# Kernel optimization log

Measured on AMD Instinct MI355X. Metric: run time of the kernel, lower is better.

Reference implementation:

```python
import jax, jax.numpy as jnp
import numpy as np

B, T, U, H = 4, 256, 64, 512
INNER, VOCAB = 512, 1024


def setup_inputs() -> dict:
    key = jax.random.key(0)
    ks = jax.random.split(key, 6)
    s_in = 1.0 / np.sqrt(2 * H)
    s_h = 1.0 / np.sqrt(INNER)
    return {
        "enc_state": jax.random.normal(ks[0], (B, T, H), dtype=jnp.float32),
        "dec_state": jax.random.normal(ks[1], (B, U, H), dtype=jnp.float32),
        "W1": jax.random.normal(ks[2], (2 * H, INNER), dtype=jnp.float32) * s_in,
        "b1": jnp.zeros((INNER,), dtype=jnp.float32),
        "W2": jax.random.normal(ks[3], (INNER, VOCAB), dtype=jnp.float32) * s_h,
        "b2": jnp.zeros((VOCAB,), dtype=jnp.float32),
    }


def reference(enc_state, dec_state, W1, b1, W2, b2):
    # JointNet: broadcast enc [B,T,1,H] and dec [B,1,U,H], concat -> Linear -> tanh -> Linear -> log_softmax
    # concat+Linear is split into two smaller matmuls (mathematically identical):
    # cat([e,d]) @ W1 == e @ W1[:H] + d @ W1[H:]
    enc_proj = jnp.einsum("bth,hi->bti", enc_state, W1[:H])      # [B,T,INNER]
    dec_proj = jnp.einsum("buh,hi->bui", dec_state, W1[H:])      # [B,U,INNER]
    hidden = jnp.tanh(enc_proj[:, :, None, :] + dec_proj[:, None, :, :] + b1)  # [B,T,U,INNER]
    logits = jnp.einsum("btui,iv->btuv", hidden, W2) + b2        # [B,T,U,VOCAB]
    return jax.nn.log_softmax(logits, axis=-1)
```

## Files before the change

kernel.cpp:

```cpp
#include <hip/hip_runtime.h>
#include <hip/hip_bf16.h>
#include <cstdint>
#include <cstddef>


typedef __attribute__((ext_vector_type(8))) short short8;
typedef __attribute__((ext_vector_type(4))) float f32x4;

#define AS_STRIDE 520
#define SMEM_A_BYTES (64 * AS_STRIDE * 2)
#define SMEM_BS_OFF SMEM_A_BYTES
#define BS_CHUNK 65536
#define SMEM_RED_OFF (SMEM_BS_OFF + BS_CHUNK)
#define SMEM_TOTAL (SMEM_RED_OFF + 16 * 64 * 4 * 2)

#define WS_EP_OFF 0
#define WS_DP_OFF (1024 * 512 * 4)
#define WS_W2_OFF (WS_DP_OFF + 256 * 512 * 4)

__device__ __forceinline__ unsigned short f2bf(float x) {
  unsigned int u = __builtin_bit_cast(unsigned int, x);
  u += 0x7FFFu + ((u >> 16) & 1u);
  return (unsigned short)(u >> 16);
}

__device__ __forceinline__ float fast_tanh(float x) {
  float ax = fabsf(x);
  float e = __expf(-2.0f * ax);
  float t = (1.0f - e) / (1.0f + e);
  return copysignf(t, x);
}

__device__ __forceinline__ void gload_lds16(const void* g, void* l) {
  __builtin_amdgcn_global_load_lds(
      (const __attribute__((address_space(1))) unsigned int*)g,
      (__attribute__((address_space(3))) unsigned int*)l, 16, 0, 0);
}

__global__ __launch_bounds__(512) void prep_proj(
    const float* __restrict__ enc, const float* __restrict__ dec,
    const float* __restrict__ W1, const float* __restrict__ b1,
    float* __restrict__ ep, float* __restrict__ dp) {
  __shared__ float As[4 * 512];
  const int tid = threadIdx.x;
  const int r0 = blockIdx.x * 4;
  const bool isenc = (r0 < 1024);
  const float* A = isenc ? (enc + (size_t)r0 * 512) : (dec + (size_t)(r0 - 1024) * 512);
  const float* W = isenc ? W1 : (W1 + 512 * 512);
  float* O = isenc ? (ep + (size_t)r0 * 512) : (dp + (size_t)(r0 - 1024) * 512);

  for (int idx = tid; idx < 4 * 512; idx += 512) As[idx] = A[idx];
  __syncthreads();

  const int c = tid;
  float acc[4] = {0.f, 0.f, 0.f, 0.f};
  const float4* As4 = (const float4*)As;
#pragma unroll 4
  for (int k4 = 0; k4 < 128; ++k4) {
    const int kb = k4 * 4;
    float w0 = W[(size_t)(kb + 0) * 512 + c];
    float w1 = W[(size_t)(kb + 1) * 512 + c];
    float w2 = W[(size_t)(kb + 2) * 512 + c];
    float w3 = W[(size_t)(kb + 3) * 512 + c];
#pragma unroll
    for (int r = 0; r < 4; ++r) {
      float4 a = As4[r * 128 + k4];
      acc[r] += a.x * w0 + a.y * w1 + a.z * w2 + a.w * w3;
    }
  }
  const float bias = isenc ? b1[c] : 0.0f;
#pragma unroll
  for (int r = 0; r < 4; ++r) O[(size_t)r * 512 + c] = acc[r] + bias;
}

__global__ __launch_bounds__(256) void prep_w2(const float* __restrict__ W2,
                                               char* __restrict__ w2st) {
  const int g = blockIdx.x * 256 + threadIdx.x;
  const int v = g & 1023;
  const int kc = g >> 10;
  unsigned short vals[32];
#pragma unroll
  for (int ki = 0; ki < 32; ++ki)
    vals[ki] = f2bf(W2[(size_t)(kc * 32 + ki) * 1024 + v]);
  uint4* dst = (uint4*)(w2st + (size_t)kc * BS_CHUNK + (size_t)v * 64);
  const uint4* s = (const uint4*)vals;
  dst[0] = s[0]; dst[1] = s[1]; dst[2] = s[2]; dst[3] = s[3];
}

__global__ __launch_bounds__(1024, 1) void joint(
    const float* __restrict__ ep, const float* __restrict__ dp,
    const char* __restrict__ w2st, const float* __restrict__ b2,
    float* __restrict__ out) {
  extern __shared__ char smem[];
  unsigned short* As = (unsigned short*)smem;
  char* Bs = smem + SMEM_BS_OFF;
  float* redM = (float*)(smem + SMEM_RED_OFF);
  float* redS = redM + 16 * 64;

  const int tid = threadIdx.x;
  const int wave = tid >> 6, lane = tid & 63;
  const int lo = lane & 15, hi = lane >> 4;
  const int wm = wave >> 3, wn = wave & 7;
  const int bt = blockIdx.x;
  const int m0 = bt * 64;
  const int dpbase = (bt >> 8) * 64;

  {
    const char* src = w2st;
#pragma unroll
    for (int r = 0; r < 4; ++r) {
      const int off = r * 16384 + tid * 16;
      gload_lds16(src + off, Bs + off);
    }
  }

  {
    const int c = tid & 511;
    const int rh = tid >> 9;
    const float e = ep[(size_t)bt * 512 + c];
#pragma unroll 4
    for (int r = 0; r < 32; ++r) {
      const int row = rh * 32 + r;
      float h = fast_tanh(e + dp[(size_t)(dpbase + row) * 512 + c]);
      As[row * AS_STRIDE + c] = f2bf(h);
    }
  }

  f32x4 acc[2][8];
#pragma unroll
  for (int mi = 0; mi < 2; ++mi)
#pragma unroll
    for (int ni = 0; ni < 8; ++ni)
#pragma unroll
      for (int j = 0; j < 4; ++j) acc[mi][ni][j] = 0.0f;

  const int nbase = wn * 128;
  const int arow0 = wm * 32 + lo;

  for (int kc = 0; kc < 16; ++kc) {
    __syncthreads();
    short8 a0 = *(const short8*)(As + (size_t)arow0 * AS_STRIDE + kc * 32 + hi * 8);
    short8 a1 = *(const short8*)(As + (size_t)(arow0 + 16) * AS_STRIDE + kc * 32 + hi * 8);
#pragma unroll
    for (int ni = 0; ni < 8; ++ni) {
      short8 b = *(const short8*)(Bs + (size_t)(nbase + ni * 16 + lo) * 64 + hi * 16);
      acc[0][ni] = __builtin_amdgcn_mfma_f32_16x16x32_bf16(a0, b, acc[0][ni], 0, 0, 0);
      acc[1][ni] = __builtin_amdgcn_mfma_f32_16x16x32_bf16(a1, b, acc[1][ni], 0, 0, 0);
    }
    if (kc < 15) {
      __syncthreads();
      const char* src = w2st + (size_t)(kc + 1) * BS_CHUNK;
#pragma unroll
      for (int r = 0; r < 4; ++r) {
        const int off = r * 16384 + tid * 16;
        gload_lds16(src + off, Bs + off);
      }
    }
  }
  __syncthreads();

  float b2v[8];
#pragma unroll
  for (int ni = 0; ni < 8; ++ni) b2v[ni] = b2[nbase + ni * 16 + lo];
#pragma unroll
  for (int mi = 0; mi < 2; ++mi)
#pragma unroll
    for (int ni = 0; ni < 8; ++ni)
#pragma unroll
      for (int j = 0; j < 4; ++j) acc[mi][ni][j] += b2v[ni];

  float pm[2][4];
#pragma unroll
  for (int mi = 0; mi < 2; ++mi)
#pragma unroll
    for (int r = 0; r < 4; ++r) {
      float m = -3.402823e38f;
#pragma unroll
      for (int ni = 0; ni < 8; ++ni) m = fmaxf(m, acc[mi][ni][r]);
      pm[mi][r] = m;
    }
#pragma unroll
  for (int off = 1; off < 16; off <<= 1)
#pragma unroll
    for (int mi = 0; mi < 2; ++mi)
#pragma unroll
      for (int r = 0; r < 4; ++r)
        pm[mi][r] = fmaxf(pm[mi][r], __shfl_xor(pm[mi][r], off));
  if (lo == 0) {
#pragma unroll
    for (int mi = 0; mi < 2; ++mi)
#pragma unroll
      for (int r = 0; r < 4; ++r)
        redM[wave * 64 + wm * 32 + mi * 16 + hi * 4 + r] = pm[mi][r];
  }
  __syncthreads();
  float rm[2][4];
#pragma unroll
  for (int mi = 0; mi < 2; ++mi)
#pragma unroll
    for (int r = 0; r < 4; ++r) {
      const int gr = wm * 32 + mi * 16 + hi * 4 + r;
      float m = redM[(wm * 8 + 0) * 64 + gr];
#pragma unroll
      for (int w = 1; w < 8; ++w) m = fmaxf(m, redM[(wm * 8 + w) * 64 + gr]);
      rm[mi][r] = m;
    }

  float ps[2][4];
#pragma unroll
  for (int mi = 0; mi < 2; ++mi)
#pragma unroll
    for (int r = 0; r < 4; ++r) {
      float s = 0.0f;
#pragma unroll
      for (int ni = 0; ni < 8; ++ni) s += __expf(acc[mi][ni][r] - rm[mi][r]);
      ps[mi][r] = s;
    }
#pragma unroll
  for (int off = 1; off < 16; off <<= 1)
#pragma unroll
    for (int mi = 0; mi < 2; ++mi)
#pragma unroll
      for (int r = 0; r < 4; ++r)
        ps[mi][r] += __shfl_xor(ps[mi][r], off);
  if (lo == 0) {
#pragma unroll
    for (int mi = 0; mi < 2; ++mi)
#pragma unroll
      for (int r = 0; r < 4; ++r)
        redS[wave * 64 + wm * 32 + mi * 16 + hi * 4 + r] = ps[mi][r];
  }
  __syncthreads();

#pragma unroll
  for (int mi = 0; mi < 2; ++mi)
#pragma unroll
    for (int r = 0; r < 4; ++r) {
      const int gr = wm * 32 + mi * 16 + hi * 4 + r;
      float s = 0.0f;
#pragma unroll
      for (int w = 0; w < 8; ++w) s += redS[(wm * 8 + w) * 64 + gr];
      const float sub = rm[mi][r] + __logf(s);
      float* op = out + (size_t)(m0 + gr) * 1024 + nbase + lo;
#pragma unroll
      for (int ni = 0; ni < 8; ++ni) op[ni * 16] = acc[mi][ni][r] - sub;
    }
}

extern "C" void kernel_launch(void* const* d_in, const int* in_sizes, int n_in,
                              void* d_out, int out_size, void* d_ws, size_t ws_size,
                              hipStream_t stream) {
  const float* enc = (const float*)d_in[0];
  const float* dec = (const float*)d_in[1];
  const float* W1  = (const float*)d_in[2];
  const float* b1  = (const float*)d_in[3];
  const float* W2  = (const float*)d_in[4];
  const float* b2  = (const float*)d_in[5];
  float* out = (float*)d_out;

  char* ws = (char*)d_ws;
  float* ep = (float*)(ws + WS_EP_OFF);
  float* dp = (float*)(ws + WS_DP_OFF);
  char* w2st = ws + WS_W2_OFF;

  prep_proj<<<320, 512, 0, stream>>>(enc, dec, W1, b1, ep, dp);
  prep_w2<<<64, 256, 0, stream>>>(W2, w2st);
  joint<<<1024, 1024, SMEM_TOTAL, stream>>>(ep, dp, w2st, b2, out);
}
```

Baseline: 215.1 us.

## Register double-buffer W2 chunks in joint kernel and merge prep kernels

The joint kernel stops using direct global-to-LDS loads. It keeps two W2 chunks in registers, prefetching chunk k+2 while chunk k is written to LDS and consumed by MFMAs, and raises wave priority during the MFMA block. The two prep kernels are merged into one launch with a block-index split, removing one kernel launch. This costs more VGPRs (32 extra registers per thread at 1024 threads/block) and adds an LDS store pass, but it should hide global latency better than the previous load-then-barrier scheme.

```diff
diff --git a/kernel.cpp b/kernel.cpp
--- a/kernel.cpp
+++ b/kernel.cpp
@@ -31,60 +31,54 @@
   return copysignf(t, x);
 }
 
-__device__ __forceinline__ void gload_lds16(const void* g, void* l) {
-  __builtin_amdgcn_global_load_lds(
-      (const __attribute__((address_space(1))) unsigned int*)g,
-      (__attribute__((address_space(3))) unsigned int*)l, 16, 0, 0);
-}
-
-__global__ __launch_bounds__(512) void prep_proj(
+__global__ __launch_bounds__(512) void prep(
     const float* __restrict__ enc, const float* __restrict__ dec,
     const float* __restrict__ W1, const float* __restrict__ b1,
-    float* __restrict__ ep, float* __restrict__ dp) {
+    const float* __restrict__ W2,
+    float* __restrict__ ep, float* __restrict__ dp, char* __restrict__ w2st) {
   __shared__ float As[4 * 512];
   const int tid = threadIdx.x;
-  const int r0 = blockIdx.x * 4;
-  const bool isenc = (r0 < 1024);
-  const float* A = isenc ? (enc + (size_t)r0 * 512) : (dec + (size_t)(r0 - 1024) * 512);
-  const float* W = isenc ? W1 : (W1 + 512 * 512);
-  float* O = isenc ? (ep + (size_t)r0 * 512) : (dp + (size_t)(r0 - 1024) * 512);
-
-  for (int idx = tid; idx < 4 * 512; idx += 512) As[idx] = A[idx];
-  __syncthreads();
-
-  const int c = tid;
-  float acc[4] = {0.f, 0.f, 0.f, 0.f};
-  const float4* As4 = (const float4*)As;
+  if (blockIdx.x < 320) {
+    const int r0 = blockIdx.x * 4;
+    const bool isenc = (r0 < 1024);
+    const float* A = isenc ? (enc + (size_t)r0 * 512) : (dec + (size_t)(r0 - 1024) * 512);
+    const float* W = isenc ? W1 : (W1 + 512 * 512);
+    float* O = isenc ? (ep + (size_t)r0 * 512) : (dp + (size_t)(r0 - 1024) * 512);
+
+    for (int idx = tid; idx < 4 * 512; idx += 512) As[idx] = A[idx];
+    __syncthreads();
+
+    const int c = tid;
+    float acc[4] = {0.f, 0.f, 0.f, 0.f};
+    const float4* As4 = (const float4*)As;
 #pragma unroll 4
-  for (int k4 = 0; k4 < 128; ++k4) {
-    const int kb = k4 * 4;
-    float w0 = W[(size_t)(kb + 0) * 512 + c];
-    float w1 = W[(size_t)(kb + 1) * 512 + c];
-    float w2 = W[(size_t)(kb + 2) * 512 + c];
-    float w3 = W[(size_t)(kb + 3) * 512 + c];
-#pragma unroll
-    for (int r = 0; r < 4; ++r) {
-      float4 a = As4[r * 128 + k4];
-      acc[r] += a.x * w0 + a.y * w1 + a.z * w2 + a.w * w3;
-    }
-  }
-  const float bias = isenc ? b1[c] : 0.0f;
-#pragma unroll
-  for (int r = 0; r < 4; ++r) O[(size_t)r * 512 + c] = acc[r] + bias;
-}
-
-__global__ __launch_bounds__(256) void prep_w2(const float* __restrict__ W2,
-                                               char* __restrict__ w2st) {
-  const int g = blockIdx.x * 256 + threadIdx.x;
-  const int v = g & 1023;
-  const int kc = g >> 10;
-  unsigned short vals[32];
-#pragma unroll
-  for (int ki = 0; ki < 32; ++ki)
-    vals[ki] = f2bf(W2[(size_t)(kc * 32 + ki) * 1024 + v]);
-  uint4* dst = (uint4*)(w2st + (size_t)kc * BS_CHUNK + (size_t)v * 64);
-  const uint4* s = (const uint4*)vals;
-  dst[0] = s[0]; dst[1] = s[1]; dst[2] = s[2]; dst[3] = s[3];
+    for (int k4 = 0; k4 < 128; ++k4) {
+      const int kb = k4 * 4;
+      float w0 = W[(size_t)(kb + 0) * 512 + c];
+      float w1 = W[(size_t)(kb + 1) * 512 + c];
+      float w2 = W[(size_t)(kb + 2) * 512 + c];
+      float w3 = W[(size_t)(kb + 3) * 512 + c];
+#pragma unroll
+      for (int r = 0; r < 4; ++r) {
+        float4 a = As4[r * 128 + k4];
+        acc[r] += a.x * w0 + a.y * w1 + a.z * w2 + a.w * w3;
+      }
+    }
+    const float bias = isenc ? b1[c] : 0.0f;
+#pragma unroll
+    for (int r = 0; r < 4; ++r) O[(size_t)r * 512 + c] = acc[r] + bias;
+  } else {
+    const int g = (blockIdx.x - 320) * 512 + tid;
+    const int v = g & 1023;
+    const int kc = g >> 10;
+    unsigned short vals[32];
+#pragma unroll
+    for (int ki = 0; ki < 32; ++ki)
+      vals[ki] = f2bf(W2[(size_t)(kc * 32 + ki) * 1024 + v]);
+    uint4* dst = (uint4*)(w2st + (size_t)kc * BS_CHUNK + (size_t)v * 64);
+    const uint4* s = (const uint4*)vals;
+    dst[0] = s[0]; dst[1] = s[1]; dst[2] = s[2]; dst[3] = s[3];
+  }
 }
 
 __global__ __launch_bounds__(1024, 1) void joint(
@@ -105,13 +99,18 @@
   const int m0 = bt * 64;
   const int dpbase = (bt >> 8) * 64;
 
+  uint4 P0, P1, P2, P3, Q0, Q1, Q2, Q3;
   {
-    const char* src = w2st;
-#pragma unroll
-    for (int r = 0; r < 4; ++r) {
-      const int off = r * 16384 + tid * 16;
-      gload_lds16(src + off, Bs + off);
-    }
+    const char* s0 = w2st;
+    const char* s1 = w2st + BS_CHUNK;
+    P0 = *(const uint4*)(s0 + 0 * 16384 + tid * 16);
+    P1 = *(const uint4*)(s0 + 1 * 16384 + tid * 16);
+    P2 = *(const uint4*)(s0 + 2 * 16384 + tid * 16);
+    P3 = *(const uint4*)(s0 + 3 * 16384 + tid * 16);
+    Q0 = *(const uint4*)(s1 + 0 * 16384 + tid * 16);
+    Q1 = *(const uint4*)(s1 + 1 * 16384 + tid * 16);
+    Q2 = *(const uint4*)(s1 + 2 * 16384 + tid * 16);
+    Q3 = *(const uint4*)(s1 + 3 * 16384 + tid * 16);
   }
 
   {
@@ -137,26 +136,48 @@
   const int nbase = wn * 128;
   const int arow0 = wm * 32 + lo;
 
-  for (int kc = 0; kc < 16; ++kc) {
-    __syncthreads();
-    short8 a0 = *(const short8*)(As + (size_t)arow0 * AS_STRIDE + kc * 32 + hi * 8);
-    short8 a1 = *(const short8*)(As + (size_t)(arow0 + 16) * AS_STRIDE + kc * 32 + hi * 8);
-#pragma unroll
-    for (int ni = 0; ni < 8; ++ni) {
-      short8 b = *(const short8*)(Bs + (size_t)(nbase + ni * 16 + lo) * 64 + hi * 16);
-      acc[0][ni] = __builtin_amdgcn_mfma_f32_16x16x32_bf16(a0, b, acc[0][ni], 0, 0, 0);
-      acc[1][ni] = __builtin_amdgcn_mfma_f32_16x16x32_bf16(a1, b, acc[1][ni], 0, 0, 0);
-    }
-    if (kc < 15) {
-      __syncthreads();
-      const char* src = w2st + (size_t)(kc + 1) * BS_CHUNK;
-#pragma unroll
-      for (int r = 0; r < 4; ++r) {
-        const int off = r * 16384 + tid * 16;
-        gload_lds16(src + off, Bs + off);
-      }
-    }
-  }
+  __syncthreads();
+
+#define K_STEP(S0, S1, S2, S3, KC, PF, NEXT)                                        \
+  {                                                                                 \
+    __builtin_amdgcn_s_barrier();              \
+    asm volatile("" ::: "memory");                                                  \
+    *(uint4*)(Bs + 0 * 16384 + tid * 16) = S0;     \
+    *(uint4*)(Bs + 1 * 16384 + tid * 16) = S1;                                      \
+    *(uint4*)(Bs + 2 * 16384 + tid * 16) = S2;                                      \
+    *(uint4*)(Bs + 3 * 16384 + tid * 16) = S3;                                      \
+    if (PF) {                                                                       \
+      const char* _src = w2st + (size_t)(NEXT)*BS_CHUNK;                            \
+      S0 = *(const uint4*)(_src + 0 * 16384 + tid * 16);                            \
+      S1 = *(const uint4*)(_src + 1 * 16384 + tid * 16);                            \
+      S2 = *(const uint4*)(_src + 2 * 16384 + tid * 16);                            \
+      S3 = *(const uint4*)(_src + 3 * 16384 + tid * 16);                            \
+    }                                                                               \
+    asm volatile("s_waitcnt lgkmcnt(0)" ::: "memory");  \
+    __builtin_amdgcn_s_barrier();                    \
+    asm volatile("" ::: "memory");                                                  \
+    __builtin_amdgcn_sched_barrier(0);                                              \
+    short8 a0 = *(const short8*)(As + (size_t)arow0 * AS_STRIDE + (KC)*32 + hi * 8);\
+    short8 a1 = *(const short8*)(As + (size_t)(arow0 + 16) * AS_STRIDE + (KC)*32 + hi * 8); \
+    __builtin_amdgcn_s_setprio(1);                                                  \
+    _Pragma("unroll")                                                               \
+    for (int ni = 0; ni < 8; ++ni) {                                                \
+      short8 b = *(const short8*)(Bs + (size_t)(nbase + ni * 16 + lo) * 64 + hi * 16); \
+      acc[0][ni] = __builtin_amdgcn_mfma_f32_16x16x32_bf16(a0, b, acc[0][ni], 0, 0, 0); \
+      acc[1][ni] = __builtin_amdgcn_mfma_f32_16x16x32_bf16(a1, b, acc[1][ni], 0, 0, 0); \
+    }                                                                               \
+    __builtin_amdgcn_s_setprio(0);                                                  \
+  }
+
+  for (int kc2 = 0; kc2 < 7; ++kc2) {
+    const int kc = kc2 * 2;
+    K_STEP(P0, P1, P2, P3, kc, 1, kc + 2);
+    K_STEP(Q0, Q1, Q2, Q3, kc + 1, 1, kc + 3);
+  }
+  K_STEP(P0, P1, P2, P3, 14, 0, 0);
+  K_STEP(Q0, Q1, Q2, Q3, 15, 0, 0);
+#undef K_STEP
+
   __syncthreads();
 
   float b2v[8];
@@ -263,7 +284,6 @@
   float* dp = (float*)(ws + WS_DP_OFF);
   char* w2st = ws + WS_W2_OFF;
 
-  prep_proj<<<320, 512, 0, stream>>>(enc, dec, W1, b1, ep, dp);
-  prep_w2<<<64, 256, 0, stream>>>(W2, w2st);
+  prep<<<352, 512, 0, stream>>>(enc, dec, W1, b1, W2, ep, dp, w2st);
   joint<<<1024, 1024, SMEM_TOTAL, stream>>>(ep, dp, w2st, b2, out);
 }
```

New measurement: 198.6 us. -7.7%, faster.

## Load W2 fragments straight to registers with prefetch, halve joint tile, merge prep kernels

Applied to the files above, without the earlier changes.

The joint kernel no longer stages W2 chunks through LDS with block-wide barriers. Each wave now loads its bf16 W2 fragments directly from global memory into registers and prefetches the next K chunk during the current MFMAs. Blocks shrink to 512 threads covering 32 rows, which cuts LDS use enough to allow several resident blocks per CU, and setprio is raised around the MFMA burst. The two prep kernels are merged into one launch. In exchange, every block re-reads all of W2 from global memory or cache, and register pressure rises from the double-buffered B fragments.

```diff
diff --git a/kernel.cpp b/kernel.cpp
--- a/kernel.cpp
+++ b/kernel.cpp
@@ -8,11 +8,7 @@
 typedef __attribute__((ext_vector_type(4))) float f32x4;
 
 #define AS_STRIDE 520
-#define SMEM_A_BYTES (64 * AS_STRIDE * 2)
-#define SMEM_BS_OFF SMEM_A_BYTES
 #define BS_CHUNK 65536
-#define SMEM_RED_OFF (SMEM_BS_OFF + BS_CHUNK)
-#define SMEM_TOTAL (SMEM_RED_OFF + 16 * 64 * 4 * 2)
 
 #define WS_EP_OFF 0
 #define WS_DP_OFF (1024 * 512 * 4)
@@ -31,98 +27,86 @@
   return copysignf(t, x);
 }
 
-__device__ __forceinline__ void gload_lds16(const void* g, void* l) {
-  __builtin_amdgcn_global_load_lds(
-      (const __attribute__((address_space(1))) unsigned int*)g,
-      (__attribute__((address_space(3))) unsigned int*)l, 16, 0, 0);
-}
-
-__global__ __launch_bounds__(512) void prep_proj(
+__global__ __launch_bounds__(512) void prep(
     const float* __restrict__ enc, const float* __restrict__ dec,
     const float* __restrict__ W1, const float* __restrict__ b1,
-    float* __restrict__ ep, float* __restrict__ dp) {
+    const float* __restrict__ W2,
+    float* __restrict__ ep, float* __restrict__ dp, char* __restrict__ w2st) {
   __shared__ float As[4 * 512];
   const int tid = threadIdx.x;
-  const int r0 = blockIdx.x * 4;
-  const bool isenc = (r0 < 1024);
-  const float* A = isenc ? (enc + (size_t)r0 * 512) : (dec + (size_t)(r0 - 1024) * 512);
-  const float* W = isenc ? W1 : (W1 + 512 * 512);
-  float* O = isenc ? (ep + (size_t)r0 * 512) : (dp + (size_t)(r0 - 1024) * 512);
-
-  for (int idx = tid; idx < 4 * 512; idx += 512) As[idx] = A[idx];
-  __syncthreads();
-
-  const int c = tid;
-  float acc[4] = {0.f, 0.f, 0.f, 0.f};
-  const float4* As4 = (const float4*)As;
+  if (blockIdx.x < 320) {
+    const int r0 = blockIdx.x * 4;
+    const bool isenc = (r0 < 1024);
+    const float* A = isenc ? (enc + (size_t)r0 * 512) : (dec + (size_t)(r0 - 1024) * 512);
+    const float* W = isenc ? W1 : (W1 + 512 * 512);
+    float* O = isenc ? (ep + (size_t)r0 * 512) : (dp + (size_t)(r0 - 1024) * 512);
+
+    for (int idx = tid; idx < 4 * 512; idx += 512) As[idx] = A[idx];
+    __syncthreads();
+
+    const int c = tid;
+    float acc[4] = {0.f, 0.f, 0.f, 0.f};
+    const float4* As4 = (const float4*)As;
 #pragma unroll 4
-  for (int k4 = 0; k4 < 128; ++k4) {
-    const int kb = k4 * 4;
-    float w0 = W[(size_t)(kb + 0) * 512 + c];
-    float w1 = W[(size_t)(kb + 1) * 512 + c];
-    float w2 = W[(size_t)(kb + 2) * 512 + c];
-    float w3 = W[(size_t)(kb + 3) * 512 + c];
-#pragma unroll
-    for (int r = 0; r < 4; ++r) {
-      float4 a = As4[r * 128 + k4];
-      acc[r] += a.x * w0 + a.y * w1 + a.z * w2 + a.w * w3;
-    }
-  }
-  const float bias = isenc ? b1[c] : 0.0f;
-#pragma unroll
-  for (int r = 0; r < 4; ++r) O[(size_t)r * 512 + c] = acc[r] + bias;
-}
-
-__global__ __launch_bounds__(256) void prep_w2(const float* __restrict__ W2,
-                                               char* __restrict__ w2st) {
-  const int g = blockIdx.x * 256 + threadIdx.x;
-  const int v = g & 1023;
-  const int kc = g >> 10;
-  unsigned short vals[32];
-#pragma unroll
-  for (int ki = 0; ki < 32; ++ki)
-    vals[ki] = f2bf(W2[(size_t)(kc * 32 + ki) * 1024 + v]);
-  uint4* dst = (uint4*)(w2st + (size_t)kc * BS_CHUNK + (size_t)v * 64);
-  const uint4* s = (const uint4*)vals;
-  dst[0] = s[0]; dst[1] = s[1]; dst[2] = s[2]; dst[3] = s[3];
-}
-
-__global__ __launch_bounds__(1024, 1) void joint(
+    for (int k4 = 0; k4 < 128; ++k4) {
+      const int kb = k4 * 4;
+      float w0 = W[(size_t)(kb + 0) * 512 + c];
+      float w1 = W[(size_t)(kb + 1) * 512 + c];
+      float w2 = W[(size_t)(kb + 2) * 512 + c];
+      float w3 = W[(size_t)(kb + 3) * 512 + c];
+#pragma unroll
+      for (int r = 0; r < 4; ++r) {
+        float4 a = As4[r * 128 + k4];
+        acc[r] += a.x * w0 + a.y * w1 + a.z * w2 + a.w * w3;
+      }
+    }
+    const float bias = isenc ? b1[c] : 0.0f;
+#pragma unroll
+    for (int r = 0; r < 4; ++r) O[(size_t)r * 512 + c] = acc[r] + bias;
+  } else {
+    const int g = (blockIdx.x - 320) * 512 + tid;
+    const int v = g & 1023;
+    const int kc = g >> 10;
+    unsigned short vals[32];
+#pragma unroll
+    for (int ki = 0; ki < 32; ++ki)
+      vals[ki] = f2bf(W2[(size_t)(kc * 32 + ki) * 1024 + v]);
+    uint4* dst = (uint4*)(w2st + (size_t)kc * BS_CHUNK + (size_t)v * 64);
+    const uint4* s = (const uint4*)vals;
+    dst[0] = s[0]; dst[1] = s[1]; dst[2] = s[2]; dst[3] = s[3];
+  }
+}
+
+__global__ __launch_bounds__(512, 4) void joint(
     const float* __restrict__ ep, const float* __restrict__ dp,
     const char* __restrict__ w2st, const float* __restrict__ b2,
     float* __restrict__ out) {
-  extern __shared__ char smem[];
-  unsigned short* As = (unsigned short*)smem;
-  char* Bs = smem + SMEM_BS_OFF;
-  float* redM = (float*)(smem + SMEM_RED_OFF);
-  float* redS = redM + 16 * 64;
+  __shared__ unsigned short As[32 * AS_STRIDE];
+  __shared__ float redM[8 * 32];
+  __shared__ float redS[8 * 32];
 
   const int tid = threadIdx.x;
   const int wave = tid >> 6, lane = tid & 63;
   const int lo = lane & 15, hi = lane >> 4;
-  const int wm = wave >> 3, wn = wave & 7;
-  const int bt = blockIdx.x;
-  const int m0 = bt * 64;
-  const int dpbase = (bt >> 8) * 64;
+  const int m0 = blockIdx.x * 32;
+  const int bt = m0 >> 6;
+  const int dprow0 = ((bt >> 8) << 6) + (m0 & 63);
+  const int nbase = wave * 128;
+
+  const char* bbase = w2st + (size_t)(nbase + lo) * 64 + hi * 16;
+
+  short8 b[8];
+#pragma unroll
+  for (int ni = 0; ni < 8; ++ni)
+    b[ni] = *(const short8*)(bbase + ni * 1024);
 
   {
-    const char* src = w2st;
-#pragma unroll
-    for (int r = 0; r < 4; ++r) {
-      const int off = r * 16384 + tid * 16;
-      gload_lds16(src + off, Bs + off);
-    }
-  }
-
-  {
-    const int c = tid & 511;
-    const int rh = tid >> 9;
+    const int c = tid;
     const float e = ep[(size_t)bt * 512 + c];
 #pragma unroll 4
     for (int r = 0; r < 32; ++r) {
-      const int row = rh * 32 + r;
-      float h = fast_tanh(e + dp[(size_t)(dpbase + row) * 512 + c]);
-      As[row * AS_STRIDE + c] = f2bf(h);
+      float h = fast_tanh(e + dp[(size_t)(dprow0 + r) * 512 + c]);
+      As[r * AS_STRIDE + c] = f2bf(h);
     }
   }
 
@@ -134,30 +118,31 @@
 #pragma unroll
       for (int j = 0; j < 4; ++j) acc[mi][ni][j] = 0.0f;
 
-  const int nbase = wn * 128;
-  const int arow0 = wm * 32 + lo;
-
+  __syncthreads();
+
+#pragma unroll
   for (int kc = 0; kc < 16; ++kc) {
-    __syncthreads();
-    short8 a0 = *(const short8*)(As + (size_t)arow0 * AS_STRIDE + kc * 32 + hi * 8);
-    short8 a1 = *(const short8*)(As + (size_t)(arow0 + 16) * AS_STRIDE + kc * 32 + hi * 8);
+    short8 bn[8];
+    if (kc < 15) {
+      const char* src = bbase + (size_t)(kc + 1) * BS_CHUNK;
+#pragma unroll
+      for (int ni = 0; ni < 8; ++ni)
+        bn[ni] = *(const short8*)(src + ni * 1024);
+    }
+    short8 a0 = *(const short8*)(As + (size_t)lo * AS_STRIDE + kc * 32 + hi * 8);
+    short8 a1 = *(const short8*)(As + (size_t)(16 + lo) * AS_STRIDE + kc * 32 + hi * 8);
+    __builtin_amdgcn_s_setprio(1);
 #pragma unroll
     for (int ni = 0; ni < 8; ++ni) {
-      short8 b = *(const short8*)(Bs + (size_t)(nbase + ni * 16 + lo) * 64 + hi * 16);
-      acc[0][ni] = __builtin_amdgcn_mfma_f32_16x16x32_bf16(a0, b, acc[0][ni], 0, 0, 0);
-      acc[1][ni] = __builtin_amdgcn_mfma_f32_16x16x32_bf16(a1, b, acc[1][ni], 0, 0, 0);
-    }
+      acc[0][ni] = __builtin_amdgcn_mfma_f32_16x16x32_bf16(a0, b[ni], acc[0][ni], 0, 0, 0);
+      acc[1][ni] = __builtin_amdgcn_mfma_f32_16x16x32_bf16(a1, b[ni], acc[1][ni], 0, 0, 0);
+    }
+    __builtin_amdgcn_s_setprio(0);
     if (kc < 15) {
-      __syncthreads();
-      const char* src = w2st + (size_t)(kc + 1) * BS_CHUNK;
-#pragma unroll
-      for (int r = 0; r < 4; ++r) {
-        const int off = r * 16384 + tid * 16;
-        gload_lds16(src + off, Bs + off);
-      }
-    }
-  }
-  __syncthreads();
+#pragma unroll
+      for (int ni = 0; ni < 8; ++ni) b[ni] = bn[ni];
+    }
+  }
 
   float b2v[8];
 #pragma unroll
@@ -191,7 +176,7 @@
     for (int mi = 0; mi < 2; ++mi)
 #pragma unroll
       for (int r = 0; r < 4; ++r)
-        redM[wave * 64 + wm * 32 + mi * 16 + hi * 4 + r] = pm[mi][r];
+        redM[wave * 32 + mi * 16 + hi * 4 + r] = pm[mi][r];
   }
   __syncthreads();
   float rm[2][4];
@@ -199,10 +184,10 @@
   for (int mi = 0; mi < 2; ++mi)
 #pragma unroll
     for (int r = 0; r < 4; ++r) {
-      const int gr = wm * 32 + mi * 16 + hi * 4 + r;
-      float m = redM[(wm * 8 + 0) * 64 + gr];
-#pragma unroll
-      for (int w = 1; w < 8; ++w) m = fmaxf(m, redM[(wm * 8 + w) * 64 + gr]);
+      const int row = mi * 16 + hi * 4 + r;
+      float m = redM[row];
+#pragma unroll
+      for (int w = 1; w < 8; ++w) m = fmaxf(m, redM[w * 32 + row]);
       rm[mi][r] = m;
     }
 
@@ -228,7 +213,7 @@
     for (int mi = 0; mi < 2; ++mi)
 #pragma unroll
       for (int r = 0; r < 4; ++r)
-        redS[wave * 64 + wm * 32 + mi * 16 + hi * 4 + r] = ps[mi][r];
+        redS[wave * 32 + mi * 16 + hi * 4 + r] = ps[mi][r];
   }
   __syncthreads();
 
@@ -236,12 +221,12 @@
   for (int mi = 0; mi < 2; ++mi)
 #pragma unroll
     for (int r = 0; r < 4; ++r) {
-      const int gr = wm * 32 + mi * 16 + hi * 4 + r;
+      const int row = mi * 16 + hi * 4 + r;
       float s = 0.0f;
 #pragma unroll
-      for (int w = 0; w < 8; ++w) s += redS[(wm * 8 + w) * 64 + gr];
+      for (int w = 0; w < 8; ++w) s += redS[w * 32 + row];
       const float sub = rm[mi][r] + __logf(s);
-      float* op = out + (size_t)(m0 + gr) * 1024 + nbase + lo;
+      float* op = out + (size_t)(m0 + row) * 1024 + nbase + lo;
 #pragma unroll
       for (int ni = 0; ni < 8; ++ni) op[ni * 16] = acc[mi][ni][r] - sub;
     }
@@ -263,7 +248,6 @@
   float* dp = (float*)(ws + WS_DP_OFF);
   char* w2st = ws + WS_W2_OFF;
 
-  prep_proj<<<320, 512, 0, stream>>>(enc, dec, W1, b1, ep, dp);
-  prep_w2<<<64, 256, 0, stream>>>(W2, w2st);
-  joint<<<1024, 1024, SMEM_TOTAL, stream>>>(ep, dp, w2st, b2, out);
-}
+  prep<<<352, 512, 0, stream>>>(enc, dec, W1, b1, W2, ep, dp, w2st);
+  joint<<<2048, 512, 0, stream>>>(ep, dp, w2st, b2, out);
+}
```

Result: slower. 359.0 us (+66.9%).
